# Optimization experiments

Measured on AMD Instinct MI355X. Metric: run time of the kernel, lower is better.

## Reference

```python
import jax, jax.numpy as jnp
import numpy as np

B, C, H, W, D = 2, 512, 16, 16, 16
GROUPS = 32
EPS = 1e-6


def setup_inputs() -> dict:
    key = jax.random.key(0)
    ks = jax.random.split(key, 6)
    s = 1.0 / np.sqrt(C)
    inp = {
        "x": jax.random.normal(ks[0], (B, C, H, W, D), jnp.float32),
        "gn_w": jnp.ones((C,), jnp.float32),
        "gn_b": jnp.zeros((C,), jnp.float32),
        "wq": jax.random.normal(ks[1], (C, C), jnp.float32) * s,
        "bq": jnp.zeros((C,), jnp.float32),
        "wk": jax.random.normal(ks[2], (C, C), jnp.float32) * s,
        "bk": jnp.zeros((C,), jnp.float32),
        "wv": jax.random.normal(ks[3], (C, C), jnp.float32) * s,
        "bv": jnp.zeros((C,), jnp.float32),
        "wp": jax.random.normal(ks[4], (C, C), jnp.float32) * s,
        "bp": jnp.zeros((C,), jnp.float32),
    }
    return inp


def reference(x, gn_w, gn_b, wq, bq, wk, bk, wv, bv, wp, bp):
    b, c, h, w, d = x.shape
    # GroupNorm(32 groups, eps=1e-6, affine)
    xg = x.reshape(b, GROUPS, c // GROUPS, h, w, d)
    mu = xg.mean(axis=(2, 3, 4, 5), keepdims=True)
    var = xg.var(axis=(2, 3, 4, 5), keepdims=True)
    hn = ((xg - mu) / jnp.sqrt(var + EPS)).reshape(b, c, h, w, d)
    hn = hn * gn_w[None, :, None, None, None] + gn_b[None, :, None, None, None]
    # 1x1x1 conv projections == per-token channel matmul
    n = h * w * d
    hf = hn.reshape(b, c, n)
    q = jnp.einsum('oc,bcn->bon', wq, hf) + bq[None, :, None]  # [b,c,n]
    k = jnp.einsum('oc,bcn->bon', wk, hf) + bk[None, :, None]
    v = jnp.einsum('oc,bcn->bon', wv, hf) + bv[None, :, None]
    # attention: scores[b,i,j] = sum_c q[b,c,i] k[b,c,j] / sqrt(c)
    scores = jnp.einsum('bci,bcj->bij', q, k) * (c ** -0.5)
    attn = jax.nn.softmax(scores, axis=2)  # [b,n,n]
    # out[b,c,i] = sum_j v[b,c,j] attn[b,i,j]
    o = jnp.einsum('bij,bcj->bci', attn, v)
    o = jnp.einsum('oc,bcn->bon', wp, o) + bp[None, :, None]
    return x + o.reshape(b, c, h, w, d)
```

## Files before the change

### kernel.cpp

```cpp
#include <hip/hip_runtime.h>
#include <hip/hip_bf16.h>
#include <stdint.h>

typedef short short8 __attribute__((ext_vector_type(8)));
typedef float f32x4  __attribute__((ext_vector_type(4)));
typedef float f32x2  __attribute__((ext_vector_type(2)));
typedef unsigned char uchar;

#define B_ 2
#define C_ 512
#define N_ 4096
#define G_ 32
#define WN (C_ * C_)
#define PREP_BLOCKS 4101

static __device__ __forceinline__ short f2bf(float f) {
    return __builtin_bit_cast(short, __float2bfloat16(f));
}
static __device__ __forceinline__ uchar f2fp8(float f) {
    return (uchar)(__builtin_amdgcn_cvt_pk_fp8_f32(f, f, 0, false) & 0xff);
}

static __device__ __forceinline__ void wg_barrier_lds() {
    __builtin_amdgcn_s_waitcnt(0xC07F);
    __builtin_amdgcn_s_barrier();
}

__global__ void prep_stats(const float* __restrict__ wq, const float* __restrict__ wk,
                           const float* __restrict__ wv, const float* __restrict__ wp,
                           const float* __restrict__ bq, const float* __restrict__ bk,
                           const float* __restrict__ x,
                           uchar* __restrict__ Wb, float* __restrict__ bqk,
                           float* __restrict__ raw) {
    if (blockIdx.x < PREP_BLOCKS) {
        int i = blockIdx.x * 256 + threadIdx.x;
        if (i < 4 * WN) {
            const float* src = (i < 2*WN) ? ((i < WN) ? wq : wk) : ((i < 3*WN) ? wv : wp);
            Wb[i] = f2fp8(src[i & (WN - 1)] * 16.f);
        } else if (i < 4*WN + 1024) {
            int j = i - 4*WN;
            bqk[j] = (j < C_) ? bq[j] : bk[j - C_];
        }
        return;
    }
    const int idx = blockIdx.x - PREP_BLOCKS;
    const int bg = idx >> 2, qt = idx & 3;
    const float4* p = (const float4*)(x + (size_t)bg * 16 * N_ + (size_t)qt * 4 * N_);
    int tid = threadIdx.x;
    float s = 0.f, sq = 0.f;
    #pragma unroll
    for (int rep = 0; rep < 16; rep++) {
        float4 t = p[rep * 256 + tid];
        s  += t.x + t.y + t.z + t.w;
        sq += t.x*t.x + t.y*t.y + t.z*t.z + t.w*t.w;
    }
    __shared__ float rs[256], rq[256];
    rs[tid] = s; rq[tid] = sq;
    __syncthreads();
    for (int h = 128; h > 0; h >>= 1) {
        if (tid < h) { rs[tid] += rs[tid+h]; rq[tid] += rq[tid+h]; }
        __syncthreads();
    }
    if (tid == 0) {
        raw[idx*2+0] = rs[0];
        raw[idx*2+1] = rq[0];
    }
}

__global__ void gn_apply(const float* __restrict__ x, const float* __restrict__ raw,
                         const float* __restrict__ gw, const float* __restrict__ gb,
                         uchar* __restrict__ hn) {
    __shared__ uchar t[64 * 68];
    const int n0 = blockIdx.x * 64, c0 = blockIdx.y * 64, b = blockIdx.z;
    const int lane = threadIdx.x & 63, w = threadIdx.x >> 6;
    const float inv = 1.f / (16.f * N_);
    #pragma unroll
    for (int rep = 0; rep < 16; rep++) {
        int c  = rep * 4 + w;
        int cc = c0 + c;
        int g  = cc >> 4;
        int base = (b*G_ + g) * 8;
        float mean = (raw[base] + raw[base+2] + raw[base+4] + raw[base+6]) * inv;
        float var  = (raw[base+1] + raw[base+3] + raw[base+5] + raw[base+7]) * inv - mean * mean;
        float rstd = rsqrtf(var + 1e-6f);
        float sc = gw[cc] * rstd;
        float bi = gb[cc] - mean * sc;
        float v = x[((size_t)(b*C_ + cc)) * N_ + n0 + lane];
        t[lane*68 + c] = f2fp8(v * sc + bi);
    }
    __syncthreads();
    #pragma unroll
    for (int rep = 0; rep < 16; rep++) {
        int n = rep * 4 + w;
        hn[((size_t)(b*N_ + n0 + n)) * C_ + c0 + lane] = t[n*68 + lane];
    }
}

template<int BM, int BIAS_MODE, int OUT_MODE, int K>
__global__ __launch_bounds__(256, 2)
void gemm_nt8(const uchar* __restrict__ A, int lda, long long sAz,
              const uchar* __restrict__ Bm, int ldb, long long sBz,
              void* __restrict__ Cv, int ldc, long long sCz,
              const float* __restrict__ bias,
              const float* __restrict__ res,
              float alpha) {
    constexpr int MI = BM / 32;
    constexpr int T  = K / 64;
    __shared__ uchar As[2][BM * 64];
    __shared__ uchar Bs[2][128 * 64];
    const int tid  = threadIdx.x;
    const int lane = tid & 63;
    const int wid  = tid >> 6;
    const int wr   = wid >> 1;
    const int wc   = wid & 1;
    const int m0 = blockIdx.y * BM;
    const int n0 = blockIdx.x * 128;
    const int z  = blockIdx.z;

    const int r = tid >> 2;
    const int c = tid & 3;
    const int wofs = r * 64 + ((c ^ ((r >> 2) & 3)) << 4);
    const bool swp = ((r >> 1) & 1) != 0;

    const uchar* Ap  = A  + sAz * z + (size_t)(m0 + r) * lda + c * 16;
    const uchar* Ap1 = Ap + (size_t)64 * lda;
    const uchar* Bp  = Bm + sBz * z + (size_t)(n0 + r) * ldb + c * 16;
    const uchar* Bp1 = Bp + (size_t)64 * ldb;

    f32x4 acc[MI][4];
    #pragma unroll
    for (int i = 0; i < MI; i++)
        #pragma unroll
        for (int j = 0; j < 4; j++)
            acc[i][j] = f32x4{0.f, 0.f, 0.f, 0.f};

    const int fm = lane & 15;
    const int q  = lane >> 4;
    const int h  = (fm >> 1) & 7;
    const int ro0 = ((q ^ h) << 3);
    const int ro1 = (((4 + q) ^ h) << 3);

    short8 ra[4][2], rb[4][2];

    #define ST16(dst, v) do { short8 _w; \
        if (swp) { _w[0]=(v)[4];_w[1]=(v)[5];_w[2]=(v)[6];_w[3]=(v)[7]; \
                   _w[4]=(v)[0];_w[5]=(v)[1];_w[6]=(v)[2];_w[7]=(v)[3]; } \
        else _w = (v); \
        *(short8*)(dst) = _w; } while (0)
    #define LOADG(s, kb) do { ra[s][0] = *(const short8*)(Ap  + (kb)); \
                              if (BM == 128) ra[s][1] = *(const short8*)(Ap1 + (kb)); \
                              rb[s][0] = *(const short8*)(Bp  + (kb)); \
                              rb[s][1] = *(const short8*)(Bp1 + (kb)); } while (0)
    #define STORES(b, s) do { ST16(&As[b][wofs], ra[s][0]); \
                              if (BM == 128) ST16(&As[b][wofs + 64*64], ra[s][1]); \
                              ST16(&Bs[b][wofs], rb[s][0]); ST16(&Bs[b][wofs + 64*64], rb[s][1]); } while (0)
    #define STEP(bt, J, DO_STORE, DO_LOAD) do { \
        long af0[MI], af1[MI], bf0[4], bf1[4]; \
        _Pragma("unroll") \
        for (int i = 0; i < MI; i++) { \
            int ar = (wr*(BM/2) + i*16 + fm) * 64; \
            af0[i] = *(const long*)&As[(J)&1][ar + ro0]; \
            af1[i] = *(const long*)&As[(J)&1][ar + ro1]; \
        } \
        _Pragma("unroll") \
        for (int i = 0; i < 4; i++) { \
            int br = (wc*64 + i*16 + fm) * 64; \
            bf0[i] = *(const long*)&Bs[(J)&1][br + ro0]; \
            bf1[i] = *(const long*)&Bs[(J)&1][br + ro1]; \
        } \
        if (DO_STORE) STORES(((J)+1)&1, ((J)+1)&3); \
        if (DO_LOAD)  LOADG(((J)+3)&3, ((bt)+(J)+3)*64); \
        _Pragma("unroll") \
        for (int mi = 0; mi < MI; mi++) \
            _Pragma("unroll") \
            for (int ni = 0; ni < 4; ni++) \
                acc[mi][ni] = __builtin_amdgcn_mfma_f32_16x16x32_fp8_fp8(af0[mi], bf0[ni], acc[mi][ni], 0, 0, 0); \
        _Pragma("unroll") \
        for (int mi = 0; mi < MI; mi++) \
            _Pragma("unroll") \
            for (int ni = 0; ni < 4; ni++) \
                acc[mi][ni] = __builtin_amdgcn_mfma_f32_16x16x32_fp8_fp8(af1[mi], bf1[ni], acc[mi][ni], 0, 0, 0); \
        wg_barrier_lds(); \
    } while (0)

    LOADG(0, 0);
    LOADG(1, 64);
    LOADG(2, 128);
    STORES(0, 0);
    wg_barrier_lds();

    for (int m = 0; m < T/4 - 1; m++) {
        const int bt = m * 4;
        STEP(bt, 0, true, true);
        STEP(bt, 1, true, true);
        STEP(bt, 2, true, true);
        STEP(bt, 3, true, true);
    }
    {
        const int bt = T - 4;
        STEP(bt, 0, true,  true);
        STEP(bt, 1, true,  false);
        STEP(bt, 2, true,  false);
        STEP(bt, 3, false, false);
    }
    #undef ST16
    #undef LOADG
    #undef STORES
    #undef STEP

    const int colb = n0 + wc*64 + fm;
    const int rowb = m0 + wr*(BM/2) + (q << 2);
    #pragma unroll
    for (int mi = 0; mi < MI; mi++) {
        #pragma unroll
        for (int ni = 0; ni < 4; ni++) {
            int cc = colb + ni*16;
            float cb = (BIAS_MODE == 1) ? bias[cc] : 0.f;
            #pragma unroll
            for (int rr4 = 0; rr4 < 4; rr4++) {
                int rr = rowb + mi*16 + rr4;
                float val = acc[mi][ni][rr4] * alpha + cb;
                if (BIAS_MODE == 2) val += bias[rr];
                long long idx = sCz * z + (long long)rr * ldc + cc;
                if (OUT_MODE == 0)      ((short*)Cv)[idx] = f2bf(val);
                else if (OUT_MODE == 2) ((float*)Cv)[idx] = val + res[idx];
                else                    ((uchar*)Cv)[idx] = f2fp8(val);
            }
        }
    }
}

__global__ void softmax_rows8(uchar* __restrict__ S) {
    const int lane = threadIdx.x & 63;
    const int wave = threadIdx.x >> 6;
    const size_t row = (size_t)blockIdx.x * 4 + wave;
    uint4* rp = (uint4*)(S + row * N_);
    uint4 d[4];
    float f[64];
    float mx = -3.0e38f;
    #pragma unroll
    for (int c = 0; c < 4; c++) {
        d[c] = rp[c * 64 + lane];
        unsigned wv[4] = {d[c].x, d[c].y, d[c].z, d[c].w};
        #pragma unroll
        for (int u = 0; u < 4; u++) {
            f32x2 lo = __builtin_amdgcn_cvt_pk_f32_fp8(wv[u], false);
            f32x2 hi = __builtin_amdgcn_cvt_pk_f32_fp8(wv[u], true);
            int b = c*16 + u*4;
            f[b+0] = lo[0]; f[b+1] = lo[1]; f[b+2] = hi[0]; f[b+3] = hi[1];
            mx = fmaxf(mx, fmaxf(fmaxf(lo[0], lo[1]), fmaxf(hi[0], hi[1])));
        }
    }
    #pragma unroll
    for (int off = 32; off > 0; off >>= 1)
        mx = fmaxf(mx, __shfl_xor(mx, off));
    float sum = 0.f;
    const float k = 0.0625f;
    #pragma unroll
    for (int j = 0; j < 64; j++) { f[j] = __expf((f[j] - mx) * k); sum += f[j]; }
    #pragma unroll
    for (int off = 32; off > 0; off >>= 1)
        sum += __shfl_xor(sum, off);
    float inv = 256.f / sum;
    #pragma unroll
    for (int c = 0; c < 4; c++) {
        unsigned wv[4];
        #pragma unroll
        for (int u = 0; u < 4; u++) {
            int b = c*16 + u*4;
            int o = 0;
            o = __builtin_amdgcn_cvt_pk_fp8_f32(f[b+0]*inv, f[b+1]*inv, o, false);
            o = __builtin_amdgcn_cvt_pk_fp8_f32(f[b+2]*inv, f[b+3]*inv, o, true);
            wv[u] = (unsigned)o;
        }
        uint4 ov; ov.x = wv[0]; ov.y = wv[1]; ov.z = wv[2]; ov.w = wv[3];
        rp[c * 64 + lane] = ov;
    }
}

extern "C" void kernel_launch(void* const* d_in, const int* in_sizes, int n_in,
                              void* d_out, int out_size, void* d_ws, size_t ws_size,
                              hipStream_t stream) {
    const float* x   = (const float*)d_in[0];
    const float* gnw = (const float*)d_in[1];
    const float* gnb = (const float*)d_in[2];
    const float* wq  = (const float*)d_in[3];
    const float* bq  = (const float*)d_in[4];
    const float* wk  = (const float*)d_in[5];
    const float* bk  = (const float*)d_in[6];
    const float* wv  = (const float*)d_in[7];
    const float* bv  = (const float*)d_in[8];
    const float* wp  = (const float*)d_in[9];
    const float* bp  = (const float*)d_in[10];
    float* out = (float*)d_out;
    char*  ws  = (char*)d_ws;

    float* raw = (float*)(ws + 0);
    float* bqk = (float*)(ws + 8192);
    uchar* Wb  = (uchar*)(ws + 65536);
    uchar* Hn  = (uchar*)(ws + (2ull  << 20));
    uchar* QK8 = (uchar*)(ws + (8ull  << 20));
    uchar* V8  = (uchar*)(ws + (16ull << 20));
    uchar* Ot8 = (uchar*)(ws + (20ull << 20));
    uchar* Sb  = (uchar*)(ws + (24ull << 20));

    prep_stats<<<PREP_BLOCKS + 256, 256, 0, stream>>>(wq, wk, wv, wp, bq, bk, x, Wb, bqk, raw);
    gn_apply<<<dim3(N_/64, C_/64, B_), 256, 0, stream>>>(x, raw, gnw, gnb, Hn);

    const long long sHn = (long long)N_ * C_;
    const long long sQK = (long long)N_ * 1024;
    const long long sV  = (long long)C_ * N_;
    const long long sS  = (long long)N_ * N_;

    gemm_nt8<128,1,3,512><<<dim3(8, 32, 2), 256, 0, stream>>>(
        Hn, C_, sHn, Wb, C_, 0, QK8, 1024, sQK, bqk, nullptr, 1.f/16.f);
    gemm_nt8<64,2,3,512><<<dim3(32, 8, 2), 256, 0, stream>>>(
        Wb + 2*WN, C_, 0, Hn, C_, sHn, V8, N_, sV, bv, nullptr, 1.f/16.f);

    const float alphaS = 0.044194173824159216f * 16.f;
    gemm_nt8<128,0,3,512><<<dim3(32, 32, 2), 256, 0, stream>>>(
        QK8, 1024, sQK, QK8 + 512, 1024, sQK, Sb, N_, sS, nullptr, nullptr, alphaS);
    softmax_rows8<<<B_*N_/4, 256, 0, stream>>>(Sb);
    gemm_nt8<64,0,3,4096><<<dim3(4, 64, 2), 256, 0, stream>>>(
        Sb, N_, sS, V8, N_, sV, Ot8, C_, sHn, nullptr, nullptr, 1.f/16.f);
    gemm_nt8<64,2,2,512><<<dim3(32, 8, 2), 256, 0, stream>>>(
        Wb + 3*WN, C_, 0, Ot8, C_, sHn, out, N_, (long long)C_*N_, bp, x, 1.f/256.f);
}
```

Measured before the change: 208.0 us.

## Use direct global-to-LDS async loads with triple buffering and XCD-aware block swizzle

New measurement: 196.7 us. -5.5%, faster.

```diff
diff --git a/kernel.cpp b/kernel.cpp
--- a/kernel.cpp
+++ b/kernel.cpp
@@ -21,9 +21,10 @@
     return (uchar)(__builtin_amdgcn_cvt_pk_fp8_f32(f, f, 0, false) & 0xff);
 }
 
-static __device__ __forceinline__ void wg_barrier_lds() {
-    __builtin_amdgcn_s_waitcnt(0xC07F);
-    __builtin_amdgcn_s_barrier();
+static __device__ __forceinline__ void async16(uchar* lds_wave_base, const uchar* g) {
+    auto l  = (__attribute__((address_space(3))) unsigned int*)(uintptr_t)(lds_wave_base);
+    auto gg = (const __attribute__((address_space(1))) unsigned int*)(g);
+    __builtin_amdgcn_global_load_lds(gg, l, 16, 0, 0);
 }
 
 __global__ void prep_stats(const float* __restrict__ wq, const float* __restrict__ wk,
@@ -96,7 +97,7 @@
     }
 }
 
-template<int BM, int BIAS_MODE, int OUT_MODE, int K>
+template<int BM, int BIAS_MODE, int OUT_MODE, int K, int SWZ>
 __global__ __launch_bounds__(256, 2)
 void gemm_nt8(const uchar* __restrict__ A, int lda, long long sAz,
               const uchar* __restrict__ Bm, int ldb, long long sBz,
@@ -106,25 +107,33 @@
               float alpha) {
     constexpr int MI = BM / 32;
     constexpr int T  = K / 64;
-    __shared__ uchar As[2][BM * 64];
-    __shared__ uchar Bs[2][128 * 64];
+    constexpr int D  = (BM == 128) ? 4 : 3;
+    constexpr unsigned WAITD = 0xF70u | D;
+    constexpr unsigned WAIT0 = 0xF70u;
+    __shared__ uchar As[3][BM * 64];
+    __shared__ uchar Bs[3][128 * 64];
+
+    int bx, by, bz;
+    if (SWZ) {
+        int fid = blockIdx.x;
+        int xcd = fid & 7, j = fid >> 3;
+        int gg = (j >> 2) * 8 + xcd;
+        bx = j & 3; by = gg & 63; bz = gg >> 6;
+    } else { bx = blockIdx.x; by = blockIdx.y; bz = blockIdx.z; }
+
     const int tid  = threadIdx.x;
     const int lane = tid & 63;
     const int wid  = tid >> 6;
     const int wr   = wid >> 1;
     const int wc   = wid & 1;
-    const int m0 = blockIdx.y * BM;
-    const int n0 = blockIdx.x * 128;
-    const int z  = blockIdx.z;
-
-    const int r = tid >> 2;
-    const int c = tid & 3;
-    const int wofs = r * 64 + ((c ^ ((r >> 2) & 3)) << 4);
-    const bool swp = ((r >> 1) & 1) != 0;
-
-    const uchar* Ap  = A  + sAz * z + (size_t)(m0 + r) * lda + c * 16;
+    const int m0 = by * BM;
+    const int n0 = bx * 128;
+
+    const int r  = tid >> 2;
+    const int gc = (tid & 3) ^ ((r >> 1) & 3);
+    const uchar* Ap  = A  + sAz * bz + (size_t)(m0 + r) * lda + gc * 16;
     const uchar* Ap1 = Ap + (size_t)64 * lda;
-    const uchar* Bp  = Bm + sBz * z + (size_t)(n0 + r) * ldb + c * 16;
+    const uchar* Bp  = Bm + sBz * bz + (size_t)(n0 + r) * ldb + gc * 16;
     const uchar* Bp1 = Bp + (size_t)64 * ldb;
 
     f32x4 acc[MI][4];
@@ -134,42 +143,32 @@
         for (int j = 0; j < 4; j++)
             acc[i][j] = f32x4{0.f, 0.f, 0.f, 0.f};
 
-    const int fm = lane & 15;
-    const int q  = lane >> 4;
-    const int h  = (fm >> 1) & 7;
-    const int ro0 = ((q ^ h) << 3);
-    const int ro1 = (((4 + q) ^ h) << 3);
-
-    short8 ra[4][2], rb[4][2];
-
-    #define ST16(dst, v) do { short8 _w; \
-        if (swp) { _w[0]=(v)[4];_w[1]=(v)[5];_w[2]=(v)[6];_w[3]=(v)[7]; \
-                   _w[4]=(v)[0];_w[5]=(v)[1];_w[6]=(v)[2];_w[7]=(v)[3]; } \
-        else _w = (v); \
-        *(short8*)(dst) = _w; } while (0)
-    #define LOADG(s, kb) do { ra[s][0] = *(const short8*)(Ap  + (kb)); \
-                              if (BM == 128) ra[s][1] = *(const short8*)(Ap1 + (kb)); \
-                              rb[s][0] = *(const short8*)(Bp  + (kb)); \
-                              rb[s][1] = *(const short8*)(Bp1 + (kb)); } while (0)
-    #define STORES(b, s) do { ST16(&As[b][wofs], ra[s][0]); \
-                              if (BM == 128) ST16(&As[b][wofs + 64*64], ra[s][1]); \
-                              ST16(&Bs[b][wofs], rb[s][0]); ST16(&Bs[b][wofs + 64*64], rb[s][1]); } while (0)
-    #define STEP(bt, J, DO_STORE, DO_LOAD) do { \
+    const int fm  = lane & 15;
+    const int q   = lane >> 4;
+    const int ro0 = (((q >> 1) ^ ((fm >> 1) & 3)) << 4) | ((q & 1) << 3);
+    const int ro1 = ro0 ^ 32;
+
+    #define ISSUE(IB, u) do { size_t _kb = (size_t)(u) * 64; \
+        async16(&As[IB][wid * 1024], Ap + _kb); \
+        if (BM == 128) async16(&As[IB][4096 + wid * 1024], Ap1 + _kb); \
+        async16(&Bs[IB][wid * 1024], Bp + _kb); \
+        async16(&Bs[IB][4096 + wid * 1024], Bp1 + _kb); } while (0)
+
+    #define STEP(B, DO_ISSUE, IB, u, DO_BAR, WIMM) do { \
         long af0[MI], af1[MI], bf0[4], bf1[4]; \
         _Pragma("unroll") \
         for (int i = 0; i < MI; i++) { \
             int ar = (wr*(BM/2) + i*16 + fm) * 64; \
-            af0[i] = *(const long*)&As[(J)&1][ar + ro0]; \
-            af1[i] = *(const long*)&As[(J)&1][ar + ro1]; \
+            af0[i] = *(const long*)&As[B][ar + ro0]; \
+            af1[i] = *(const long*)&As[B][ar + ro1]; \
         } \
         _Pragma("unroll") \
         for (int i = 0; i < 4; i++) { \
             int br = (wc*64 + i*16 + fm) * 64; \
-            bf0[i] = *(const long*)&Bs[(J)&1][br + ro0]; \
-            bf1[i] = *(const long*)&Bs[(J)&1][br + ro1]; \
+            bf0[i] = *(const long*)&Bs[B][br + ro0]; \
+            bf1[i] = *(const long*)&Bs[B][br + ro1]; \
         } \
-        if (DO_STORE) STORES(((J)+1)&1, ((J)+1)&3); \
-        if (DO_LOAD)  LOADG(((J)+3)&3, ((bt)+(J)+3)*64); \
+        if (DO_ISSUE) ISSUE(IB, u); \
         _Pragma("unroll") \
         for (int mi = 0; mi < MI; mi++) \
             _Pragma("unroll") \
@@ -180,32 +179,30 @@
             _Pragma("unroll") \
             for (int ni = 0; ni < 4; ni++) \
                 acc[mi][ni] = __builtin_amdgcn_mfma_f32_16x16x32_fp8_fp8(af1[mi], bf1[ni], acc[mi][ni], 0, 0, 0); \
-        wg_barrier_lds(); \
+        if (DO_BAR) { __builtin_amdgcn_s_waitcnt(WIMM); __builtin_amdgcn_s_barrier(); } \
     } while (0)
 
-    LOADG(0, 0);
-    LOADG(1, 64);
-    LOADG(2, 128);
-    STORES(0, 0);
-    wg_barrier_lds();
-
-    for (int m = 0; m < T/4 - 1; m++) {
-        const int bt = m * 4;
-        STEP(bt, 0, true, true);
-        STEP(bt, 1, true, true);
-        STEP(bt, 2, true, true);
-        STEP(bt, 3, true, true);
-    }
-    {
-        const int bt = T - 4;
-        STEP(bt, 0, true,  true);
-        STEP(bt, 1, true,  false);
-        STEP(bt, 2, true,  false);
-        STEP(bt, 3, false, false);
-    }
-    #undef ST16
-    #undef LOADG
-    #undef STORES
+    ISSUE(0, 0);
+    ISSUE(1, 1);
+    __builtin_amdgcn_s_waitcnt(WAITD);
+    __builtin_amdgcn_s_barrier();
+
+    constexpr int Gm = (T - 2) / 3;
+    for (int m = 0; m < Gm; m++) {
+        STEP(0, 1, 2, m*3 + 2, 1, WAITD);
+        STEP(1, 1, 0, m*3 + 3, 1, WAITD);
+        STEP(2, 1, 1, m*3 + 4, 1, WAITD);
+    }
+    if (T - 3*Gm == 2) {
+        STEP(0, 0, 0, 0, 1, WAIT0);
+        STEP(1, 0, 0, 0, 0, 0);
+    } else {
+        STEP(0, 1, 2, T-2, 1, WAITD);
+        STEP(1, 1, 0, T-1, 1, WAITD);
+        STEP(2, 0, 0, 0, 1, WAIT0);
+        STEP(0, 0, 0, 0, 0, 0);
+    }
+    #undef ISSUE
     #undef STEP
 
     const int colb = n0 + wc*64 + fm;
@@ -221,7 +218,7 @@
                 int rr = rowb + mi*16 + rr4;
                 float val = acc[mi][ni][rr4] * alpha + cb;
                 if (BIAS_MODE == 2) val += bias[rr];
-                long long idx = sCz * z + (long long)rr * ldc + cc;
+                long long idx = sCz * bz + (long long)rr * ldc + cc;
                 if (OUT_MODE == 0)      ((short*)Cv)[idx] = f2bf(val);
                 else if (OUT_MODE == 2) ((float*)Cv)[idx] = val + res[idx];
                 else                    ((uchar*)Cv)[idx] = f2fp8(val);
@@ -312,17 +309,17 @@
     const long long sV  = (long long)C_ * N_;
     const long long sS  = (long long)N_ * N_;
 
-    gemm_nt8<128,1,3,512><<<dim3(8, 32, 2), 256, 0, stream>>>(
+    gemm_nt8<128,1,3,512,0><<<dim3(8, 32, 2), 256, 0, stream>>>(
         Hn, C_, sHn, Wb, C_, 0, QK8, 1024, sQK, bqk, nullptr, 1.f/16.f);
-    gemm_nt8<64,2,3,512><<<dim3(32, 8, 2), 256, 0, stream>>>(
+    gemm_nt8<64,2,3,512,0><<<dim3(32, 8, 2), 256, 0, stream>>>(
         Wb + 2*WN, C_, 0, Hn, C_, sHn, V8, N_, sV, bv, nullptr, 1.f/16.f);
 
     const float alphaS = 0.044194173824159216f * 16.f;
-    gemm_nt8<128,0,3,512><<<dim3(32, 32, 2), 256, 0, stream>>>(
+    gemm_nt8<128,0,3,512,0><<<dim3(32, 32, 2), 256, 0, stream>>>(
         QK8, 1024, sQK, QK8 + 512, 1024, sQK, Sb, N_, sS, nullptr, nullptr, alphaS);
     softmax_rows8<<<B_*N_/4, 256, 0, stream>>>(Sb);
-    gemm_nt8<64,0,3,4096><<<dim3(4, 64, 2), 256, 0, stream>>>(
+    gemm_nt8<64,0,3,4096,1><<<512, 256, 0, stream>>>(
         Sb, N_, sS, V8, N_, sV, Ot8, C_, sHn, nullptr, nullptr, 1.f/16.f);
-    gemm_nt8<64,2,2,512><<<dim3(32, 8, 2), 256, 0, stream>>>(
+    gemm_nt8<64,2,2,512,0><<<dim3(32, 8, 2), 256, 0, stream>>>(
         Wb + 3*WN, C_, 0, Ot8, C_, sHn, out, N_, (long long)C_*N_, bp, x, 1.f/256.f);
 }
```
